# Performance work log

Measured on AMD Instinct MI355X. Metric: run time of the kernel, lower is better.

## Reference

```python
import jax, jax.numpy as jnp
import numpy as np

N_NODES = 50000
N_EDGES = 1_600_000
IN_DIM, OUT_DIM, N_HEADS = 256, 64, 4
EPS = 1e-12  # F.normalize eps


def setup_inputs() -> dict:
    key = jax.random.key(0)
    k1, k2, k3, k4, k5 = jax.random.split(key, 5)
    h = jax.random.normal(k1, (N_NODES, IN_DIM), dtype=jnp.float32)
    edge_index = jax.random.randint(k2, (2, N_EDGES), 0, N_NODES, dtype=jnp.int32)
    # small scale keeps exp(leaky_relu(.)) well-conditioned (mimics xavier init)
    W = jax.random.normal(k3, (IN_DIM, OUT_DIM), dtype=jnp.float32) * 0.05
    Wl = jax.random.normal(k4, (N_HEADS, OUT_DIM), dtype=jnp.float32) * 0.05
    Wr = jax.random.normal(k5, (N_HEADS, OUT_DIM), dtype=jnp.float32) * 0.05
    b = jnp.zeros((OUT_DIM,), dtype=jnp.float32)
    return {"h": h, "W": W, "Wl": Wl, "Wr": Wr, "b": b, "edge_index": edge_index}


def reference(h, W, Wl, Wr, b, edge_index):
    N = h.shape[0]
    H = Wl.shape[0]
    x = h @ W                      # [N, D]
    el = x @ Wl.T                  # [N, H]
    er = x @ Wr.T                  # [N, H]
    src, dst = edge_index[0], edge_index[1]
    e = el[src] + er[dst]          # [E, H]
    e = jnp.exp(jax.nn.leaky_relu(e, negative_slope=0.2))
    # L1 row normalization over edges == F.normalize(dense_scatter, p=1, dim=-1)
    rowsum = jax.ops.segment_sum(e, src, num_segments=N)          # [N, H]
    w = e / jnp.maximum(rowsum, EPS)[src]                          # [E, H]
    # SpMM aggregation, per head to bound peak memory
    heads = [jax.ops.segment_sum(w[:, hd:hd + 1] * x[dst], src, num_segments=N)
             for hd in range(H)]
    out = jnp.stack(heads, axis=1)                                 # [N, H, D]
    out = jax.nn.elu(out + b)
    return out.reshape(N, H * x.shape[1])                          # [N, H*D]
```

## Files before the change

### kernel.cpp

```cpp
#include <hip/hip_runtime.h>
#include <hip/hip_bf16.h>
#include <hip/hip_fp16.h>

#define N_NODES 50000
#define N_EDGES 1600000
#define NPB    50
#define NBUK   1000
#define NSL    8
#define BCAPS  320
#define BCAPH  1280
#define GEMMB  782
#define PARTB  512
#define CHUNK  3125
#define BD     8

typedef __attribute__((ext_vector_type(8))) short short8;
typedef __attribute__((ext_vector_type(4))) float f32x4;

__device__ __forceinline__ unsigned short f2bf(float f) {
  union { float f; unsigned int i; } v; v.f = f;
  unsigned int i = v.i;
  unsigned int r = i + 0x7FFFu + ((i >> 16) & 1u);
  return (unsigned short)(r >> 16);
}

__global__ __launch_bounds__(256) void k_xpart(const float* __restrict__ hmat,
    const float* __restrict__ Wmat,
    const float* __restrict__ Wl, const float* __restrict__ Wr,
    float* __restrict__ el, float* __restrict__ er,
    __half* __restrict__ x16,
    const int* __restrict__ ei, int* __restrict__ bcnt,
    unsigned int* __restrict__ raw) {
  __shared__ __align__(16) char smem[36864];
  const int t = threadIdx.x;
  if (blockIdx.x >= PARTB) {
    unsigned short* Wt = (unsigned short*)smem;
    for (int idx = t; idx < 64 * 256; idx += 256) {
      int k = idx >> 6, n = idx & 63;
      Wt[n * 264 + k] = f2bf(Wmat[idx]);
    }
    __syncthreads();
    const int wave = t >> 6, lane = t & 63;
    const int quad = lane >> 4, l16 = lane & 15;
    const int m0 = (blockIdx.x - PARTB) * 64 + wave * 16;
    int arow = m0 + l16; if (arow >= N_NODES) arow = N_NODES - 1;
    f32x4 c[4] = {{0,0,0,0},{0,0,0,0},{0,0,0,0},{0,0,0,0}};
    const float* aptr = hmat + (size_t)arow * 256 + quad * 8;
    #pragma unroll
    for (int kb = 0; kb < 8; ++kb) {
      f32x4 a0 = *(const f32x4*)(aptr + kb * 32);
      f32x4 a1 = *(const f32x4*)(aptr + kb * 32 + 4);
      short8 a;
      a[0] = (short)f2bf(a0[0]); a[1] = (short)f2bf(a0[1]);
      a[2] = (short)f2bf(a0[2]); a[3] = (short)f2bf(a0[3]);
      a[4] = (short)f2bf(a1[0]); a[5] = (short)f2bf(a1[1]);
      a[6] = (short)f2bf(a1[2]); a[7] = (short)f2bf(a1[3]);
      #pragma unroll
      for (int nt = 0; nt < 4; ++nt) {
        int n = nt * 16 + l16;
        short8 b = *(const short8*)(&Wt[n * 264 + kb * 32 + quad * 8]);
        c[nt] = __builtin_amdgcn_mfma_f32_16x16x32_bf16(a, b, c[nt], 0, 0, 0);
      }
    }
    float wlv[4][4], wrv[4][4];
    #pragma unroll
    for (int h = 0; h < 4; ++h)
      #pragma unroll
      for (int nt = 0; nt < 4; ++nt) {
        wlv[h][nt] = Wl[h * 64 + nt * 16 + l16];
        wrv[h][nt] = Wr[h * 64 + nt * 16 + l16];
      }
    #pragma unroll
    for (int r = 0; r < 4; ++r) {
      const int grow = m0 + quad * 4 + r;
      const bool ok = grow < N_NODES;
      #pragma unroll
      for (int nt = 0; nt < 4; ++nt)
        if (ok) x16[grow * 64 + nt * 16 + l16] = __float2half(c[nt][r]);
      #pragma unroll
      for (int h = 0; h < 4; ++h) {
        float pl = c[0][r] * wlv[h][0];
        pl = fmaf(c[1][r], wlv[h][1], pl);
        pl = fmaf(c[2][r], wlv[h][2], pl);
        pl = fmaf(c[3][r], wlv[h][3], pl);
        float pr = c[0][r] * wrv[h][0];
        pr = fmaf(c[1][r], wrv[h][1], pr);
        pr = fmaf(c[2][r], wrv[h][2], pr);
        pr = fmaf(c[3][r], wrv[h][3], pr);
        #pragma unroll
        for (int off = 1; off < 16; off <<= 1) {
          pl += __shfl_xor(pl, off, 64);
          pr += __shfl_xor(pr, off, 64);
        }
        if (ok && l16 == 0) { el[grow * 4 + h] = pl; er[grow * 4 + h] = pr; }
      }
    }
  } else {
    int* scnt = (int*)smem;
    unsigned int* sbin = (unsigned int*)(smem + 4000);
    const int pj = blockIdx.x;
    const int slice = blockIdx.x & 7;
    for (int i = t; i < NBUK; i += 256) scnt[i] = 0;
    __syncthreads();
    const int e0 = pj * CHUNK;
    for (int e = e0 + t; e < e0 + CHUNK; e += 256) {
      int s = ei[e], d = ei[N_EDGES + e];
      int b = s / NPB;
      int sl = s - b * NPB;
      unsigned int val = ((unsigned int)d << 8) | (unsigned int)sl;
      int p = atomicAdd(&scnt[b], 1);
      if (p < BD) {
        sbin[b * BD + p] = val;
      } else {
        int cell = b * NSL + slice;
        int gp = atomicAdd(&bcnt[cell * 16], 1);
        if (gp < BCAPS) raw[(size_t)cell * BCAPS + gp] = val;
      }
    }
    __syncthreads();
    for (int b = t; b < NBUK; b += 256) {
      int c = scnt[b]; if (c > BD) c = BD;
      if (c > 0) {
        int cell = b * NSL + slice;
        int gp = atomicAdd(&bcnt[cell * 16], c);
        for (int k = 0; k < c; ++k) {
          int idx = gp + k;
          if (idx < BCAPS) raw[(size_t)cell * BCAPS + idx] = sbin[b * BD + k];
        }
      }
    }
  }
}

__global__ __launch_bounds__(256) void k_bucket(const unsigned int* __restrict__ raw,
    const int* __restrict__ bcnt,
    const float* __restrict__ el, const float* __restrict__ er,
    int4* __restrict__ recs, int* __restrict__ rs_s, int* __restrict__ rs_e) {
  __shared__ unsigned int sraw[BCAPH];
  __shared__ int pref[NPB + 1];
  __shared__ int cur[NPB];
  const int b = blockIdx.x >> 1, H = blockIdx.x & 1, t = threadIdx.x;
  const int s0 = H * 4;
  int c0 = bcnt[(b * NSL + s0 + 0) * 16]; if (c0 > BCAPS) c0 = BCAPS;
  int c1 = bcnt[(b * NSL + s0 + 1) * 16]; if (c1 > BCAPS) c1 = BCAPS;
  int c2 = bcnt[(b * NSL + s0 + 2) * 16]; if (c2 > BCAPS) c2 = BCAPS;
  int c3 = bcnt[(b * NSL + s0 + 3) * 16]; if (c3 > BCAPS) c3 = BCAPS;
  const int o1 = c0, o2 = c0 + c1, o3 = c0 + c1 + c2, cnt = o3 + c3;
  if (t <= NPB) pref[t] = 0;
  __syncthreads();
  for (int j = t; j < c0; j += 256) { unsigned int r = raw[(size_t)(b*NSL+s0+0)*BCAPS + j]; sraw[j]      = r; atomicAdd(&pref[(int)(r & 255u) + 1], 1); }
  for (int j = t; j < c1; j += 256) { unsigned int r = raw[(size_t)(b*NSL+s0+1)*BCAPS + j]; sraw[o1 + j] = r; atomicAdd(&pref[(int)(r & 255u) + 1], 1); }
  for (int j = t; j < c2; j += 256) { unsigned int r = raw[(size_t)(b*NSL+s0+2)*BCAPS + j]; sraw[o2 + j] = r; atomicAdd(&pref[(int)(r & 255u) + 1], 1); }
  for (int j = t; j < c3; j += 256) { unsigned int r = raw[(size_t)(b*NSL+s0+3)*BCAPS + j]; sraw[o3 + j] = r; atomicAdd(&pref[(int)(r & 255u) + 1], 1); }
  __syncthreads();
  if (t == 0) {
    int run = 0;
    #pragma unroll
    for (int n = 0; n <= NPB; ++n) { run += pref[n]; pref[n] = run; }
  }
  __syncthreads();
  const int wbase = (b * 2 + H) * BCAPH;
  if (t < NPB) {
    cur[t] = pref[t];
    rs_s[H * N_NODES + b * NPB + t] = wbase + pref[t];
    rs_e[H * N_NODES + b * NPB + t] = wbase + pref[t + 1];
  }
  __syncthreads();
  const int base = b * NPB;
  for (int j = t; j < cnt; j += 256) {
    unsigned int r = sraw[j];
    int sl = (int)(r & 255u);
    int d  = (int)(r >> 8);
    int pos = atomicAdd(&cur[sl], 1);
    f32x4 a = ((const f32x4*)el)[base + sl];
    f32x4 e = ((const f32x4*)er)[d];
    float w[4];
    #pragma unroll
    for (int hh = 0; hh < 4; ++hh) {
      float tt = a[hh] + e[hh];
      tt = (tt >= 0.f) ? tt : 0.2f * tt;
      w[hh] = __expf(tt);
    }
    union { __half2 h; int i; } u01, u23;
    u01.h = __floats2half2_rn(w[0], w[1]);
    u23.h = __floats2half2_rn(w[2], w[3]);
    int4 rc; rc.x = d; rc.y = u01.i; rc.z = u23.i; rc.w = 0;
    recs[(size_t)wbase + pos] = rc;
  }
}

__global__ __launch_bounds__(256) void k_agg(const __half* __restrict__ x16,
    const int* __restrict__ rs_s, const int* __restrict__ rs_e,
    const int4* __restrict__ recs,
    const float* __restrict__ bvec, float* __restrict__ out) {
  const int node = (blockIdx.x * 256 + threadIdx.x) >> 6;
  const int lane = threadIdx.x & 63;
  if (node >= N_NODES) return;
  float n0 = 0.f, n1 = 0.f, n2 = 0.f, n3 = 0.f;
  float d0 = 0.f, d1 = 0.f, d2 = 0.f, d3 = 0.f;
  #pragma unroll
  for (int hf = 0; hf < 2; ++hf) {
    const int j0 = __builtin_amdgcn_readfirstlane(rs_s[hf * N_NODES + node]);
    const int j1 = __builtin_amdgcn_readfirstlane(rs_e[hf * N_NODES + node]);
    #pragma unroll 4
    for (int j = j0; j < j1; ++j) {
      int4 rec = recs[j];
      union { int i; __half2 h; } u01, u23;
      u01.i = rec.y; u23.i = rec.z;
      float2 f01 = __half22float2(u01.h);
      float2 f23 = __half22float2(u23.h);
      const __half* rowp = x16 + ((size_t)rec.x << 6);
      float xv = __half2float(rowp[lane]);
      d0 += f01.x; d1 += f01.y; d2 += f23.x; d3 += f23.y;
      n0 = fmaf(f01.x, xv, n0); n1 = fmaf(f01.y, xv, n1);
      n2 = fmaf(f23.x, xv, n2); n3 = fmaf(f23.y, xv, n3);
    }
  }
  float bv = bvec[lane];
  size_t ob = (size_t)node * 256 + lane;
  float o;
  o = n0 / fmaxf(d0, 1e-12f) + bv; o = (o > 0.f) ? o : (__expf(o) - 1.f); out[ob      ] = o;
  o = n1 / fmaxf(d1, 1e-12f) + bv; o = (o > 0.f) ? o : (__expf(o) - 1.f); out[ob +  64] = o;
  o = n2 / fmaxf(d2, 1e-12f) + bv; o = (o > 0.f) ? o : (__expf(o) - 1.f); out[ob + 128] = o;
  o = n3 / fmaxf(d3, 1e-12f) + bv; o = (o > 0.f) ? o : (__expf(o) - 1.f); out[ob + 192] = o;
}

extern "C" void kernel_launch(void* const* d_in, const int* in_sizes, int n_in,
                              void* d_out, int out_size, void* d_ws, size_t ws_size,
                              hipStream_t stream) {
  const float* h  = (const float*)d_in[0];
  const float* W  = (const float*)d_in[1];
  const float* Wl = (const float*)d_in[2];
  const float* Wr = (const float*)d_in[3];
  const float* b  = (const float*)d_in[4];
  const int*   ei = (const int*)d_in[5];
  float* out = (float*)d_out;

  char* ws = (char*)d_ws;
  float*        el   = (float*)       (ws + 0);
  float*        er   = (float*)       (ws + 800000);
  int*          bcnt = (int*)         (ws + 1600000);
  unsigned int* raw  = (unsigned int*)(ws + 2112000);
  int4*         recs = (int4*)        (ws + 12352000);
  int*          rs_s = (int*)         (ws + 53312000);
  int*          rs_e = (int*)         (ws + 53712000);
  __half*       x16  = (__half*)      (ws + 54112000);
  (void)ws_size; (void)in_sizes; (void)n_in; (void)out_size;

  hipMemsetAsync(bcnt, 0, 512000, stream);

  k_xpart  <<<PARTB + GEMMB, 256, 0, stream>>>(h, W, Wl, Wr, el, er, x16, ei, bcnt, raw);
  k_bucket <<<2000,  256, 0, stream>>>(raw, bcnt, el, er, recs, rs_s, rs_e);
  k_agg    <<<12500, 256, 0, stream>>>(x16, rs_s, rs_e, recs, b, out);
}
```

Before: 221.9 us.

## Recompute edge attention weights in aggregation instead of storing per-edge records

The bucketing kernel now writes only the destination index per edge (4 bytes) rather than a 16-byte record holding the index plus four fp16 attention weights. The aggregation kernel loads el once per node and, for each edge, gathers er[dst] and recomputes the leaky-relu and exp. This cuts the write and read traffic of the edge records and keeps the weights in fp32. In exchange every lane of the 64-wide wave redundantly gathers er and evaluates four exps per edge.

```diff
diff --git a/kernel.cpp b/kernel.cpp
--- a/kernel.cpp
+++ b/kernel.cpp
@@ -134,8 +134,7 @@
 
 __global__ __launch_bounds__(256) void k_bucket(const unsigned int* __restrict__ raw,
     const int* __restrict__ bcnt,
-    const float* __restrict__ el, const float* __restrict__ er,
-    int4* __restrict__ recs, int* __restrict__ rs_s, int* __restrict__ rs_e) {
+    int* __restrict__ dlist, int* __restrict__ rs_s, int* __restrict__ rs_e) {
   __shared__ unsigned int sraw[BCAPH];
   __shared__ int pref[NPB + 1];
   __shared__ int cur[NPB];
@@ -166,36 +165,24 @@
     rs_e[H * N_NODES + b * NPB + t] = wbase + pref[t + 1];
   }
   __syncthreads();
-  const int base = b * NPB;
   for (int j = t; j < cnt; j += 256) {
     unsigned int r = sraw[j];
     int sl = (int)(r & 255u);
     int d  = (int)(r >> 8);
     int pos = atomicAdd(&cur[sl], 1);
-    f32x4 a = ((const f32x4*)el)[base + sl];
-    f32x4 e = ((const f32x4*)er)[d];
-    float w[4];
-    #pragma unroll
-    for (int hh = 0; hh < 4; ++hh) {
-      float tt = a[hh] + e[hh];
-      tt = (tt >= 0.f) ? tt : 0.2f * tt;
-      w[hh] = __expf(tt);
-    }
-    union { __half2 h; int i; } u01, u23;
-    u01.h = __floats2half2_rn(w[0], w[1]);
-    u23.h = __floats2half2_rn(w[2], w[3]);
-    int4 rc; rc.x = d; rc.y = u01.i; rc.z = u23.i; rc.w = 0;
-    recs[(size_t)wbase + pos] = rc;
+    dlist[wbase + pos] = d;
   }
 }
 
 __global__ __launch_bounds__(256) void k_agg(const __half* __restrict__ x16,
     const int* __restrict__ rs_s, const int* __restrict__ rs_e,
-    const int4* __restrict__ recs,
+    const int* __restrict__ dlist,
+    const float* __restrict__ el, const float* __restrict__ er,
     const float* __restrict__ bvec, float* __restrict__ out) {
   const int node = (blockIdx.x * 256 + threadIdx.x) >> 6;
   const int lane = threadIdx.x & 63;
   if (node >= N_NODES) return;
+  const f32x4 ea = ((const f32x4*)el)[node];
   float n0 = 0.f, n1 = 0.f, n2 = 0.f, n3 = 0.f;
   float d0 = 0.f, d1 = 0.f, d2 = 0.f, d3 = 0.f;
   #pragma unroll
@@ -204,16 +191,18 @@
     const int j1 = __builtin_amdgcn_readfirstlane(rs_e[hf * N_NODES + node]);
     #pragma unroll 4
     for (int j = j0; j < j1; ++j) {
-      int4 rec = recs[j];
-      union { int i; __half2 h; } u01, u23;
-      u01.i = rec.y; u23.i = rec.z;
-      float2 f01 = __half22float2(u01.h);
-      float2 f23 = __half22float2(u23.h);
-      const __half* rowp = x16 + ((size_t)rec.x << 6);
+      const int dd = dlist[j];
+      const f32x4 ev = ((const f32x4*)er)[dd];
+      const __half* rowp = x16 + ((size_t)dd << 6);
       float xv = __half2float(rowp[lane]);
-      d0 += f01.x; d1 += f01.y; d2 += f23.x; d3 += f23.y;
-      n0 = fmaf(f01.x, xv, n0); n1 = fmaf(f01.y, xv, n1);
-      n2 = fmaf(f23.x, xv, n2); n3 = fmaf(f23.y, xv, n3);
+      float t0 = ea[0] + ev[0]; t0 = (t0 >= 0.f) ? t0 : 0.2f * t0;
+      float t1 = ea[1] + ev[1]; t1 = (t1 >= 0.f) ? t1 : 0.2f * t1;
+      float t2 = ea[2] + ev[2]; t2 = (t2 >= 0.f) ? t2 : 0.2f * t2;
+      float t3 = ea[3] + ev[3]; t3 = (t3 >= 0.f) ? t3 : 0.2f * t3;
+      float w0 = __expf(t0), w1 = __expf(t1), w2 = __expf(t2), w3 = __expf(t3);
+      d0 += w0; d1 += w1; d2 += w2; d3 += w3;
+      n0 = fmaf(w0, xv, n0); n1 = fmaf(w1, xv, n1);
+      n2 = fmaf(w2, xv, n2); n3 = fmaf(w3, xv, n3);
     }
   }
   float bv = bvec[lane];
@@ -237,19 +226,19 @@
   float* out = (float*)d_out;
 
   char* ws = (char*)d_ws;
-  float*        el   = (float*)       (ws + 0);
-  float*        er   = (float*)       (ws + 800000);
-  int*          bcnt = (int*)         (ws + 1600000);
-  unsigned int* raw  = (unsigned int*)(ws + 2112000);
-  int4*         recs = (int4*)        (ws + 12352000);
-  int*          rs_s = (int*)         (ws + 53312000);
-  int*          rs_e = (int*)         (ws + 53712000);
-  __half*       x16  = (__half*)      (ws + 54112000);
+  float*        el    = (float*)       (ws + 0);
+  float*        er    = (float*)       (ws + 800000);
+  int*          bcnt  = (int*)         (ws + 1600000);
+  unsigned int* raw   = (unsigned int*)(ws + 2112000);
+  int*          dlist = (int*)         (ws + 12352000);
+  int*          rs_s  = (int*)         (ws + 22592000);
+  int*          rs_e  = (int*)         (ws + 22992000);
+  __half*       x16   = (__half*)      (ws + 23392000);
   (void)ws_size; (void)in_sizes; (void)n_in; (void)out_size;
 
   hipMemsetAsync(bcnt, 0, 512000, stream);
 
   k_xpart  <<<PARTB + GEMMB, 256, 0, stream>>>(h, W, Wl, Wr, el, er, x16, ei, bcnt, raw);
-  k_bucket <<<2000,  256, 0, stream>>>(raw, bcnt, el, er, recs, rs_s, rs_e);
-  k_agg    <<<12500, 256, 0, stream>>>(x16, rs_s, rs_e, recs, b, out);
-}
+  k_bucket <<<2000,  256, 0, stream>>>(raw, bcnt, dlist, rs_s, rs_e);
+  k_agg    <<<12500, 256, 0, stream>>>(x16, rs_s, rs_e, dlist, el, er, b, out);
+}
```

Result: slower. 249.0 us (+12.2%).
